# Optimization experiments

Measured on AMD Instinct MI355X. Metric: run time of the kernel, lower is better.

## Reference

```python
import jax, jax.numpy as jnp
import numpy as np

N, E, IN, OUT = 50000, 800000, 256, 256
EPS = 1e-5


def setup_inputs() -> dict:
    key = jax.random.key(0)
    k1, k2, k3 = jax.random.split(key, 3)
    x = jax.random.normal(k1, (N, IN), dtype=jnp.float32)
    edge_index = jax.random.randint(k2, (2, E), 0, N, dtype=jnp.int64)
    batch = jnp.zeros((N,), dtype=jnp.int64)
    # glorot-style init for GCN weight
    scale = jnp.sqrt(2.0 / (IN + OUT)).astype(jnp.float32)
    W = jax.random.normal(k3, (IN, OUT), dtype=jnp.float32) * scale
    conv_bias = jnp.zeros((OUT,), dtype=jnp.float32)
    ln_weight = jnp.ones((OUT,), dtype=jnp.float32)
    ln_bias = jnp.zeros((OUT,), dtype=jnp.float32)
    prelu_a = jnp.full((1,), 0.25, dtype=jnp.float32)  # nn.PReLU default
    return {"x": x, "edge_index": edge_index, "batch": batch, "W": W,
            "conv_bias": conv_bias, "ln_weight": ln_weight,
            "ln_bias": ln_bias, "prelu_a": prelu_a}


def reference(x, edge_index, batch, W, conv_bias, ln_weight, ln_bias, prelu_a):
    n = x.shape[0]
    src, dst = edge_index[0], edge_index[1]
    # GCNConv: add self-loops, symmetric deg^{-1/2} normalization
    loop = jnp.arange(n, dtype=src.dtype)
    src_f = jnp.concatenate([src, loop])  # [E+N]
    dst_f = jnp.concatenate([dst, loop])
    h = x @ W  # [N, OUT] -- transform before propagate (PyG order)
    deg = jax.ops.segment_sum(jnp.ones_like(dst_f, dtype=h.dtype), dst_f,
                              num_segments=n)  # >=1 due to self loops
    dinv = jax.lax.rsqrt(deg)
    norm = dinv[src_f] * dinv[dst_f]  # [E+N]
    out = jax.ops.segment_sum(h[src_f] * norm[:, None], dst_f,
                              num_segments=n) + conv_bias  # [N, OUT]
    # PyG LayerNorm, mode='graph', batch=None: normalize over ALL nodes+feats
    mu = out.mean()
    xc = out - mu
    std = jnp.sqrt((xc * xc).mean())
    y = xc / (std + EPS) * ln_weight + ln_bias
    # PReLU (single shared slope)
    return jnp.where(y >= 0, y, prelu_a * y)
```

## Files before the change

### kernel.cpp

```cpp
#include <hip/hip_runtime.h>
#include <hip/hip_bf16.h>


#define F 256
#define EPSV 1e-5f

typedef __attribute__((ext_vector_type(8))) short short8;
typedef __attribute__((ext_vector_type(4))) float f32x4;

__device__ __forceinline__ unsigned short f2bf(float f) {
  union { float f; unsigned u; } v; v.f = f;
  unsigned r = v.u + 0x7fffu + ((v.u >> 16) & 1u);
  return (unsigned short)(r >> 16);
}

__device__ __forceinline__ float bf2f(unsigned short u) {
  union { unsigned u; float f; } v; v.u = ((unsigned)u) << 16; return v.f;
}


__global__ void count_rank(const int* __restrict__ dst, int* __restrict__ deg_cnt,
                           int* __restrict__ rank, int E, int eb,
                           const float* __restrict__ W, unsigned short* __restrict__ Wb) {
  if ((int)blockIdx.x < eb) {
    int e = blockIdx.x * 256 + threadIdx.x;
    if (e < E) rank[e] = atomicAdd(&deg_cnt[dst[e]], 1);
    return;
  }
  int gid = (blockIdx.x - eb) * 256 + threadIdx.x;
  int j = gid & 7;
  int lane = (gid >> 3) & 63;
  int kc = (gid >> 9) & 7;
  int tt = gid >> 12;
  int k = kc * 32 + (lane >> 4) * 8 + j;
  int n = tt * 16 + (lane & 15);
  Wb[gid] = f2bf(W[k * 256 + n]);
}


__global__ void block_sums(const int* __restrict__ deg_cnt, int* __restrict__ bsum,
                           float* __restrict__ dinv, int N) {
  __shared__ int s[256];
  int t = threadIdx.x;
  int i = blockIdx.x * 256 + t;
  int d = (i < N) ? deg_cnt[i] : 0;
  if (i < N) dinv[i] = rsqrtf((float)(d + 1));
  s[t] = d;
  __syncthreads();
  for (int off = 128; off > 0; off >>= 1) {
    if (t < off) s[t] += s[t + off];
    __syncthreads();
  }
  if (t == 0) bsum[blockIdx.x] = s[0];
}

__global__ void scan_bsums(const int* __restrict__ bsum, int* __restrict__ boff, int nb) {
  __shared__ int s[256];
  int t = threadIdx.x;
  int v = (t < nb) ? bsum[t] : 0;
  s[t] = v;
  __syncthreads();
  for (int off = 1; off < 256; off <<= 1) {
    int x = (t >= off) ? s[t - off] : 0;
    __syncthreads();
    s[t] += x;
    __syncthreads();
  }
  if (t < nb) boff[t] = s[t] - v;
}

__global__ void write_csr(const int* __restrict__ deg_cnt, const int* __restrict__ boff,
                          int* __restrict__ csr_ptr, int N, int E) {
  __shared__ int s[256];
  int t = threadIdx.x;
  int i = blockIdx.x * 256 + t;
  int v = (i < N) ? deg_cnt[i] : 0;
  s[t] = v;
  __syncthreads();
  for (int off = 1; off < 256; off <<= 1) {
    int x = (t >= off) ? s[t - off] : 0;
    __syncthreads();
    s[t] += x;
    __syncthreads();
  }
  if (i < N) csr_ptr[i] = boff[blockIdx.x] + s[t] - v;
  if (i == 0) csr_ptr[N] = E;
}


__global__ void fill_gemm(const int* __restrict__ src, const int* __restrict__ dst,
                          const int* __restrict__ rank, const int* __restrict__ csr_ptr,
                          int* __restrict__ csr_src, int E, int eb,
                          const float* __restrict__ x, const unsigned short* __restrict__ Wb,
                          const float* __restrict__ dinv, ushort4* __restrict__ hb, int N) {
  __shared__ unsigned short lds[16][264];

  if ((int)blockIdx.x < eb) {
    int e = blockIdx.x * 256 + threadIdx.x;
    if (e < E) {
      int d = dst[e];
      csr_src[csr_ptr[d] + rank[e]] = src[e];
    }
    return;
  }

  int bid = blockIdx.x - eb;
  int lane = threadIdx.x & 63;
  int wave = threadIdx.x >> 6;
  int m0 = bid * 16;
  int q = lane >> 4;

  int row = m0 + (lane & 15);
  int rowc = row < N ? row : N - 1;

  f32x4 acc[4] = {{0,0,0,0},{0,0,0,0},{0,0,0,0},{0,0,0,0}};

  for (int kc = 0; kc < 8; ++kc) {
    int koff = kc * 32 + q * 8;
    const float4* xp = (const float4*)(x + (size_t)rowc * F + koff);
    float4 a0 = xp[0];
    float4 a1 = xp[1];
    short8 a;
    a[0] = f2bf(a0.x); a[1] = f2bf(a0.y); a[2] = f2bf(a0.z); a[3] = f2bf(a0.w);
    a[4] = f2bf(a1.x); a[5] = f2bf(a1.y); a[6] = f2bf(a1.z); a[7] = f2bf(a1.w);
#pragma unroll
    for (int tt = 0; tt < 4; ++tt) {
      const short8 b = *(const short8*)(Wb + (((wave * 4 + tt) * 8 + kc) * 64 + lane) * 8);
      acc[tt] = __builtin_amdgcn_mfma_f32_16x16x32_bf16(a, b, acc[tt], 0, 0, 0);
    }
  }

  int crow = q * 4;
  int ccol = lane & 15;
#pragma unroll
  for (int rr = 0; rr < 4; ++rr) {
    int orow = m0 + crow + rr;
    float dv = (orow < N) ? dinv[orow] : 0.f;
#pragma unroll
    for (int tt = 0; tt < 4; ++tt) {
      lds[crow + rr][wave * 64 + tt * 16 + ccol] = f2bf(acc[tt][rr] * dv);
    }
  }
  __syncthreads();
  int t = threadIdx.x;
  int lrow = t >> 4;
  int grow = m0 + lrow;
  if (grow < N) {
#pragma unroll
    for (int it = 0; it < 4; ++it) {
      int c4 = (t & 15) + 16 * it;
      ushort4 u = *(const ushort4*)&lds[lrow][c4 * 4];
      hb[(size_t)grow * 64 + c4] = u;
    }
  }
}


__global__ void aggregate(const ushort4* __restrict__ hb, const int* __restrict__ csr_ptr,
                          const int* __restrict__ csr_src, const float* __restrict__ dinv,
                          const float* __restrict__ conv_bias, float4* __restrict__ out,
                          double2* __restrict__ partials, int N) {
  int wave = threadIdx.x >> 6;
  int lane = threadIdx.x & 63;
  int row = blockIdx.x * 4 + wave;
  float s1 = 0.f, s2 = 0.f;

  if (row < N) {
    float di = dinv[row];
    int b0 = csr_ptr[row], b1 = csr_ptr[row + 1];
    ushort4 self = hb[(size_t)row * 64 + lane];
    float4 acc;
    acc.x = bf2f(self.x); acc.y = bf2f(self.y);
    acc.z = bf2f(self.z); acc.w = bf2f(self.w);

    for (int e = b0; e < b1; e += 16) {
      int idx[16];
#pragma unroll
      for (int j = 0; j < 16; ++j) {
        int ee = e + j;
        idx[j] = csr_src[ee < b1 ? ee : b1 - 1];
      }
      ushort4 v[16];
#pragma unroll
      for (int j = 0; j < 16; ++j) v[j] = hb[(size_t)idx[j] * 64 + lane];
#pragma unroll
      for (int j = 0; j < 16; ++j) {
        float m = (e + j < b1) ? 1.f : 0.f;
        acc.x = fmaf(bf2f(v[j].x), m, acc.x);
        acc.y = fmaf(bf2f(v[j].y), m, acc.y);
        acc.z = fmaf(bf2f(v[j].z), m, acc.z);
        acc.w = fmaf(bf2f(v[j].w), m, acc.w);
      }
    }

    float4 b = *(const float4*)(conv_bias + lane * 4);
    acc.x = fmaf(acc.x, di, b.x);
    acc.y = fmaf(acc.y, di, b.y);
    acc.z = fmaf(acc.z, di, b.z);
    acc.w = fmaf(acc.w, di, b.w);
    out[(size_t)row * 64 + lane] = acc;
    s1 = acc.x + acc.y + acc.z + acc.w;
    s2 = acc.x * acc.x + acc.y * acc.y + acc.z * acc.z + acc.w * acc.w;
  }

  __shared__ float r1[256];
  __shared__ float r2[256];
  int t = threadIdx.x;
  r1[t] = s1;
  r2[t] = s2;
  __syncthreads();
  for (int off = 128; off > 0; off >>= 1) {
    if (t < off) { r1[t] += r1[t + off]; r2[t] += r2[t + off]; }
    __syncthreads();
  }
  if (t == 0) {
    double2 pp;
    pp.x = (double)r1[0];
    pp.y = (double)r2[0];
    partials[blockIdx.x] = pp;
  }
}

__global__ void finalize_stats(const double2* __restrict__ partials, int nb,
                               float* __restrict__ stats, double cnt) {
  __shared__ double q1[1024];
  __shared__ double q2[1024];
  int t = threadIdx.x;
  double a1 = 0.0, a2 = 0.0;
  for (int i = t; i < nb; i += 1024) {
    double2 pp = partials[i];
    a1 += pp.x;
    a2 += pp.y;
  }
  q1[t] = a1;
  q2[t] = a2;
  __syncthreads();
  for (int off = 512; off > 0; off >>= 1) {
    if (t < off) { q1[t] += q1[t + off]; q2[t] += q2[t + off]; }
    __syncthreads();
  }
  if (t == 0) {
    double mu = q1[0] / cnt;
    double var = q2[0] / cnt - mu * mu;
    if (var < 0) var = 0;
    double sd = sqrt(var);
    stats[0] = (float)mu;
    stats[1] = (float)(1.0 / (sd + (double)EPSV));
  }
}

__global__ void norm_prelu(float4* __restrict__ out, const float* __restrict__ stats,
                           const float* __restrict__ lw, const float* __restrict__ lb,
                           const float* __restrict__ pa, int n4) {
  int i = blockIdx.x * blockDim.x + threadIdx.x;
  if (i >= n4) return;
  float mu = stats[0];
  float inv = stats[1];
  float a = pa[0];
  int c4 = (i & 63) * 4;
  float4 w = *(const float4*)(lw + c4);
  float4 b = *(const float4*)(lb + c4);
  float4 v = out[i];
  float y0 = (v.x - mu) * inv * w.x + b.x;
  float y1 = (v.y - mu) * inv * w.y + b.y;
  float y2 = (v.z - mu) * inv * w.z + b.z;
  float y3 = (v.w - mu) * inv * w.w + b.w;
  v.x = y0 >= 0.f ? y0 : a * y0;
  v.y = y1 >= 0.f ? y1 : a * y1;
  v.z = y2 >= 0.f ? y2 : a * y2;
  v.w = y3 >= 0.f ? y3 : a * y3;
  out[i] = v;
}


extern "C" void kernel_launch(void* const* d_in, const int* in_sizes, int n_in,
                              void* d_out, int out_size, void* d_ws, size_t ws_size,
                              hipStream_t stream) {
  const float* x = (const float*)d_in[0];
  const int* eidx = (const int*)d_in[1];
  const float* W = (const float*)d_in[3];
  const float* conv_bias = (const float*)d_in[4];
  const float* ln_w = (const float*)d_in[5];
  const float* ln_b = (const float*)d_in[6];
  const float* prelu_a = (const float*)d_in[7];
  float* out = (float*)d_out;

  int N = in_sizes[0] / F;
  int E = in_sizes[1] / 2;
  const int* src = eidx;
  const int* dst = eidx + E;

  int nAggBlocks = (N + 3) / 4;
  int eb = (E + 255) / 256;
  int gemmb = (N + 15) / 16;
  int NB = (N + 255) / 256;

  char* p = (char*)d_ws;
  auto carve = [&](size_t bytes) { char* r = p; p += (bytes + 255) & ~(size_t)255; return r; };
  ushort4* hb    = (ushort4*)carve((size_t)N * 64 * sizeof(ushort4));
  unsigned short* Wb = (unsigned short*)carve((size_t)F * F * sizeof(short));
  int* deg_cnt   = (int*)carve((size_t)N * sizeof(int));
  int* rank      = (int*)carve((size_t)E * sizeof(int));
  float* dinv    = (float*)carve((size_t)N * sizeof(float));
  int* csr_ptr   = (int*)carve((size_t)(N + 1) * sizeof(int));
  int* csr_src   = (int*)carve((size_t)E * sizeof(int));
  int* bsum      = (int*)carve((size_t)NB * sizeof(int));
  int* boff      = (int*)carve((size_t)NB * sizeof(int));
  double2* partials = (double2*)carve((size_t)nAggBlocks * sizeof(double2));
  float* stats   = (float*)carve(2 * sizeof(float));

  hipMemsetAsync(deg_cnt, 0, (size_t)N * sizeof(int), stream);

  count_rank<<<eb + 256, 256, 0, stream>>>(dst, deg_cnt, rank, E, eb, W, Wb);
  block_sums<<<NB, 256, 0, stream>>>(deg_cnt, bsum, dinv, N);
  scan_bsums<<<1, 256, 0, stream>>>(bsum, boff, NB);
  write_csr<<<NB, 256, 0, stream>>>(deg_cnt, boff, csr_ptr, N, E);
  fill_gemm<<<eb + gemmb, 256, 0, stream>>>(src, dst, rank, csr_ptr, csr_src, E, eb,
                                            x, Wb, dinv, hb, N);
  aggregate<<<nAggBlocks, 256, 0, stream>>>(hb, csr_ptr, csr_src, dinv,
                                            conv_bias, (float4*)out, partials, N);
  finalize_stats<<<1, 1024, 0, stream>>>(partials, nAggBlocks, stats,
                                         (double)N * (double)F);
  int n4 = N * (F / 4);
  norm_prelu<<<(n4 + 255) / 256, 256, 0, stream>>>((float4*)out, stats, ln_w, ln_b, prelu_a, n4);
}
```

Before: 294.3 us.

## Stage 64-row bf16 x tiles in LDS and reuse each W fragment across four row tiles

The fused GEMM path now handles 64 rows per block instead of 16. It loads and converts the x tile to bf16 into shared memory with coalesced float4 reads, then has each wave issue four MFMAs per W fragment load. This amortizes the W fragment global reads across four times as many rows and replaces strided per-lane x reads with coalesced ones. The cost is more accumulator registers (16 f32x4), a larger LDS footprint, and a quarter as many GEMM blocks.

```diff
diff --git a/kernel.cpp b/kernel.cpp
--- a/kernel.cpp
+++ b/kernel.cpp
@@ -93,7 +93,7 @@
                           int* __restrict__ csr_src, int E, int eb,
                           const float* __restrict__ x, const unsigned short* __restrict__ Wb,
                           const float* __restrict__ dinv, ushort4* __restrict__ hb, int N) {
-  __shared__ unsigned short lds[16][264];
+  __shared__ unsigned short A[64][264];
 
   if ((int)blockIdx.x < eb) {
     int e = blockIdx.x * 256 + threadIdx.x;
@@ -105,53 +105,71 @@
   }
 
   int bid = blockIdx.x - eb;
-  int lane = threadIdx.x & 63;
-  int wave = threadIdx.x >> 6;
-  int m0 = bid * 16;
+  int m0 = bid * 64;
+  int t = threadIdx.x;
+  int lane = t & 63;
+  int wave = t >> 6;
   int q = lane >> 4;
 
-  int row = m0 + (lane & 15);
-  int rowc = row < N ? row : N - 1;
-
-  f32x4 acc[4] = {{0,0,0,0},{0,0,0,0},{0,0,0,0},{0,0,0,0}};
-
+#pragma unroll
+  for (int j = 0; j < 16; ++j) {
+    int idx = j * 256 + t;
+    int row = idx >> 6;
+    int c4 = idx & 63;
+    int gr = m0 + row;
+    int grc = gr < N ? gr : N - 1;
+    float4 v = *(const float4*)(x + (size_t)grc * F + c4 * 4);
+    ushort4 u;
+    u.x = f2bf(v.x); u.y = f2bf(v.y); u.z = f2bf(v.z); u.w = f2bf(v.w);
+    *(ushort4*)&A[row][c4 * 4] = u;
+  }
+  __syncthreads();
+
+  f32x4 acc[4][4];
+#pragma unroll
+  for (int m = 0; m < 4; ++m)
+#pragma unroll
+    for (int tt = 0; tt < 4; ++tt)
+      acc[m][tt] = (f32x4){0.f, 0.f, 0.f, 0.f};
+
+  int arow = lane & 15;
   for (int kc = 0; kc < 8; ++kc) {
-    int koff = kc * 32 + q * 8;
-    const float4* xp = (const float4*)(x + (size_t)rowc * F + koff);
-    float4 a0 = xp[0];
-    float4 a1 = xp[1];
-    short8 a;
-    a[0] = f2bf(a0.x); a[1] = f2bf(a0.y); a[2] = f2bf(a0.z); a[3] = f2bf(a0.w);
-    a[4] = f2bf(a1.x); a[5] = f2bf(a1.y); a[6] = f2bf(a1.z); a[7] = f2bf(a1.w);
+    short8 a[4];
+#pragma unroll
+    for (int m = 0; m < 4; ++m)
+      a[m] = *(const short8*)&A[m * 16 + arow][kc * 32 + q * 8];
 #pragma unroll
     for (int tt = 0; tt < 4; ++tt) {
       const short8 b = *(const short8*)(Wb + (((wave * 4 + tt) * 8 + kc) * 64 + lane) * 8);
-      acc[tt] = __builtin_amdgcn_mfma_f32_16x16x32_bf16(a, b, acc[tt], 0, 0, 0);
+#pragma unroll
+      for (int m = 0; m < 4; ++m)
+        acc[m][tt] = __builtin_amdgcn_mfma_f32_16x16x32_bf16(a[m], b, acc[m][tt], 0, 0, 0);
     }
   }
 
-  int crow = q * 4;
+  __syncthreads();
+
   int ccol = lane & 15;
 #pragma unroll
-  for (int rr = 0; rr < 4; ++rr) {
-    int orow = m0 + crow + rr;
-    float dv = (orow < N) ? dinv[orow] : 0.f;
-#pragma unroll
-    for (int tt = 0; tt < 4; ++tt) {
-      lds[crow + rr][wave * 64 + tt * 16 + ccol] = f2bf(acc[tt][rr] * dv);
+  for (int m = 0; m < 4; ++m) {
+#pragma unroll
+    for (int rr = 0; rr < 4; ++rr) {
+      int lrow = m * 16 + q * 4 + rr;
+      int orow = m0 + lrow;
+      float dv = (orow < N) ? dinv[orow] : 0.f;
+#pragma unroll
+      for (int tt = 0; tt < 4; ++tt)
+        A[lrow][(wave * 4 + tt) * 16 + ccol] = f2bf(acc[m][tt][rr] * dv);
     }
   }
   __syncthreads();
-  int t = threadIdx.x;
-  int lrow = t >> 4;
-  int grow = m0 + lrow;
-  if (grow < N) {
-#pragma unroll
-    for (int it = 0; it < 4; ++it) {
-      int c4 = (t & 15) + 16 * it;
-      ushort4 u = *(const ushort4*)&lds[lrow][c4 * 4];
-      hb[(size_t)grow * 64 + c4] = u;
-    }
+#pragma unroll
+  for (int j = 0; j < 16; ++j) {
+    int idx = j * 256 + t;
+    int row = idx >> 6;
+    int c4 = idx & 63;
+    int grow = m0 + row;
+    if (grow < N) hb[(size_t)grow * 64 + c4] = *(const ushort4*)&A[row][c4 * 4];
   }
 }
 
@@ -292,7 +310,7 @@
 
   int nAggBlocks = (N + 3) / 4;
   int eb = (E + 255) / 256;
-  int gemmb = (N + 15) / 16;
+  int gemmb = (N + 63) / 64;
   int NB = (N + 255) / 256;
 
   char* p = (char*)d_ws;
```

New measurement: 273.6 us. 1.08x faster.
